# Optimization experiments

Hardware: AMD Instinct MI355X
Metric: run time of the kernel (lower is better)

## Reference

```python
import jax, jax.numpy as jnp
import numpy as np

B, CH, T, D = 16, 64, 2048, 1  # d must be 1 (tf.squeeze(x, axis=-1))
F = 8  # conv filters


def setup_inputs() -> dict:
    key = jax.random.key(0)
    k1, k2, k3, k4 = jax.random.split(key, 4)
    return {
        "x": jax.random.normal(k1, (B, CH, T, D), dtype=jnp.float32),
        "w1": jax.random.normal(k2, (D, F), dtype=jnp.float32) * 0.1,
        "b1": jnp.zeros((F,), dtype=jnp.float32),
        "w2": jax.random.normal(k3, (D, F), dtype=jnp.float32) * 0.1,
        "b2": jnp.zeros((F,), dtype=jnp.float32),
        "gamma": jax.random.normal(k4, (1,), dtype=jnp.float32) * 0.1,
    }


def reference(x, w1, b1, w2, b2, gamma):
    b, ch, t, d = x.shape
    # 1x1 Conv2D == per-position matmul over channel dim; then Permute((2,1,3)) + Reshape((t,-1))
    q = (jnp.matmul(x, w1) + b1)  # (b, ch, t, F)
    k = (jnp.matmul(x, w2) + b2)  # (b, ch, t, F)
    q = jnp.transpose(q, (0, 2, 1, 3)).reshape(b, t, ch * q.shape[-1])  # (b, t, ch*F)
    k = jnp.transpose(k, (0, 2, 1, 3)).reshape(b, t, ch * k.shape[-1])  # (b, t, ch*F)
    energy = jnp.einsum('btf,bsf->bts', q, k)  # (b, t, t)
    max_h = jnp.max(energy, axis=2, keepdims=True)
    min_h = jnp.min(energy, axis=2, keepdims=True)
    energy = (energy - min_h) / (max_h - min_h + 1e-8)
    attention = jax.nn.softmax(energy, axis=-1)  # (b, t, t)
    x_sq = x[..., 0]  # (b, ch, t)
    # matmul(x_sq, attention, transpose_b=True): out[b,c,i] = sum_j x_sq[b,c,j] * attention[b,i,j]
    mixed = jnp.einsum('bcj,bij->bci', x_sq, attention)  # (b, ch, t)
    return gamma[0] * mixed[..., None] + x  # (b, ch, t, 1)
```

## Files before the change

### kernel.cpp

```cpp
#include <hip/hip_runtime.h>

#define NB 16
#define NCH 64
#define NT 2048
#define TI 64
#define TJ 64
#define STR 72

typedef __attribute__((ext_vector_type(8))) short bf8;
typedef __attribute__((ext_vector_type(4))) float f4;

static __device__ __forceinline__ short f2b(float f) {
    unsigned u = __float_as_uint(f);
    u += 0x7fffu + ((u >> 16) & 1u);
    return (short)(u >> 16);
}

__global__ __launch_bounds__(256)
void prep_k(const float* __restrict__ x, float* __restrict__ Xs, short* __restrict__ xT) {
    __shared__ float T[NCH][65];
    const int b = blockIdx.y, t0 = blockIdx.x * 64;
    const int tid = threadIdx.x;
    const float* xb = x + (size_t)b * NCH * NT;

    const int tt = (tid & 15) * 4;
    #pragma unroll
    for (int co = 0; co < 4; ++co) {
        int c = co * 16 + (tid >> 4);
        float4 v = *reinterpret_cast<const float4*>(&xb[(size_t)c * NT + t0 + tt]);
        T[c][tt] = v.x; T[c][tt + 1] = v.y; T[c][tt + 2] = v.z; T[c][tt + 3] = v.w;
    }
    __syncthreads();
    if (tid < 64) {
        float s = 0.f;
        #pragma unroll
        for (int c = 0; c < NCH; ++c) s += T[c][tid];
        Xs[b * NT + t0 + tid] = s;
    }
    const int row = tid >> 2, cs = (tid & 3) * 16;
    bf8 v0, v1;
    #pragma unroll
    for (int u = 0; u < 8; ++u) v0[u] = f2b(T[cs + u][row]);
    #pragma unroll
    for (int u = 0; u < 8; ++u) v1[u] = f2b(T[cs + 8 + u][row]);
    short* dst = xT + ((size_t)b * NT + t0 + row) * NCH + cs;
    *reinterpret_cast<bf8*>(dst) = v0;
    *reinterpret_cast<bf8*>(dst + 8) = v1;
}

__global__ __launch_bounds__(256)
void attn2_k(const float* __restrict__ x,
             const float* __restrict__ w1, const float* __restrict__ b1p,
             const float* __restrict__ w2, const float* __restrict__ b2p,
             const float* __restrict__ gp,
             const float* __restrict__ Xs, const short* __restrict__ xT,
             float* __restrict__ out) {
    __shared__ short xiT[TI][STR];
    __shared__ short xjT[TJ][STR];
    __shared__ short xjn[NCH][STR];
    __shared__ short P[TI][STR];
    __shared__ float XjL[TJ];
    __shared__ float rowSumL[TI];

    const int b  = blockIdx.y;
    const int i0 = blockIdx.x * TI;
    const int tid  = threadIdx.x;
    const int wid  = tid >> 6;
    const int lane = tid & 63;
    const int lq   = lane >> 4;
    const int ln   = lane & 15;

    float s11 = 0.f, s1b2 = 0.f, s2b1 = 0.f, sbb = 0.f;
    #pragma unroll
    for (int f = 0; f < 8; ++f) {
        s11  += w1[f] * w2[f];
        s1b2 += w1[f] * b2p[f];
        s2b1 += b1p[f] * w2[f];
        sbb  += b1p[f] * b2p[f];
    }
    const float c0 = (float)NCH * sbb;
    const float g  = gp[0];

    const short* xTb = xT + (size_t)b * NT * NCH;
    const float* xb  = x + (size_t)b * NCH * NT;

    {
        const int row = tid >> 2, cs = (tid & 3) * 16;
        const bf8* src = reinterpret_cast<const bf8*>(xTb + (size_t)(i0 + row) * NCH + cs);
        bf8* dst = reinterpret_cast<bf8*>(&xiT[row][cs]);
        dst[0] = src[0];
        dst[1] = src[1];
    }

    float XiV[4];
    #pragma unroll
    for (int r = 0; r < 4; ++r) XiV[r] = Xs[b * NT + i0 + wid * 16 + lq * 4 + r];

    float rmin[4], rmax[4];
    #pragma unroll
    for (int r = 0; r < 4; ++r) { rmin[r] = 3.0e38f; rmax[r] = -3.0e38f; }

    for (int j0 = 0; j0 < NT; j0 += TJ) {
        __syncthreads();
        {
            const int row = tid >> 2, cs = (tid & 3) * 16;
            const bf8* src = reinterpret_cast<const bf8*>(xTb + (size_t)(j0 + row) * NCH + cs);
            bf8* dst = reinterpret_cast<bf8*>(&xjT[row][cs]);
            dst[0] = src[0];
            dst[1] = src[1];
        }
        if (tid < 16)
            reinterpret_cast<float4*>(XjL)[tid] =
                reinterpret_cast<const float4*>(Xs + b * NT + j0)[tid];
        __syncthreads();

        bf8 a0 = *reinterpret_cast<const bf8*>(&xiT[wid * 16 + ln][lq * 8]);
        bf8 a1 = *reinterpret_cast<const bf8*>(&xiT[wid * 16 + ln][32 + lq * 8]);
        #pragma unroll
        for (int nb = 0; nb < 4; ++nb) {
            bf8 bb0 = *reinterpret_cast<const bf8*>(&xjT[nb * 16 + ln][lq * 8]);
            bf8 bb1 = *reinterpret_cast<const bf8*>(&xjT[nb * 16 + ln][32 + lq * 8]);
            f4 gacc = {0.f, 0.f, 0.f, 0.f};
            gacc = __builtin_amdgcn_mfma_f32_16x16x32_bf16(a0, bb0, gacc, 0, 0, 0);
            gacc = __builtin_amdgcn_mfma_f32_16x16x32_bf16(a1, bb1, gacc, 0, 0, 0);
            const float xjv = XjL[nb * 16 + ln];
            #pragma unroll
            for (int r = 0; r < 4; ++r) {
                float e = fmaf(s11, gacc[r], fmaf(s1b2, XiV[r], fmaf(s2b1, xjv, c0)));
                rmin[r] = fminf(rmin[r], e);
                rmax[r] = fmaxf(rmax[r], e);
            }
        }
    }

    #pragma unroll
    for (int d = 1; d < 16; d <<= 1) {
        #pragma unroll
        for (int r = 0; r < 4; ++r) {
            rmin[r] = fminf(rmin[r], __shfl_xor(rmin[r], d, 64));
            rmax[r] = fmaxf(rmax[r], __shfl_xor(rmax[r], d, 64));
        }
    }
    float mn[4], inv[4];
    #pragma unroll
    for (int r = 0; r < 4; ++r) {
        mn[r]  = rmin[r];
        inv[r] = 1.f / (rmax[r] - rmin[r] + 1e-8f);
    }

    f4 macc[4];
    #pragma unroll
    for (int nb = 0; nb < 4; ++nb) macc[nb] = (f4){0.f, 0.f, 0.f, 0.f};
    float ps[4] = {0.f, 0.f, 0.f, 0.f};

    for (int j0 = 0; j0 < NT; j0 += TJ) {
        __syncthreads();
        {
            const int row = tid >> 2, cs = (tid & 3) * 16;
            const bf8* src = reinterpret_cast<const bf8*>(xTb + (size_t)(j0 + row) * NCH + cs);
            bf8* dst = reinterpret_cast<bf8*>(&xjT[row][cs]);
            dst[0] = src[0];
            dst[1] = src[1];
        }
        {
            const int c = tid >> 2, js = (tid & 3) * 16;
            const float* s = &xb[(size_t)c * NT + j0 + js];
            float4 f0 = *reinterpret_cast<const float4*>(s);
            float4 f1 = *reinterpret_cast<const float4*>(s + 4);
            float4 fA = *reinterpret_cast<const float4*>(s + 8);
            float4 fB = *reinterpret_cast<const float4*>(s + 12);
            bf8 v0, v1;
            v0[0] = f2b(f0.x); v0[1] = f2b(f0.y); v0[2] = f2b(f0.z); v0[3] = f2b(f0.w);
            v0[4] = f2b(f1.x); v0[5] = f2b(f1.y); v0[6] = f2b(f1.z); v0[7] = f2b(f1.w);
            v1[0] = f2b(fA.x); v1[1] = f2b(fA.y); v1[2] = f2b(fA.z); v1[3] = f2b(fA.w);
            v1[4] = f2b(fB.x); v1[5] = f2b(fB.y); v1[6] = f2b(fB.z); v1[7] = f2b(fB.w);
            *reinterpret_cast<bf8*>(&xjn[c][js])     = v0;
            *reinterpret_cast<bf8*>(&xjn[c][js + 8]) = v1;
        }
        if (tid < 16)
            reinterpret_cast<float4*>(XjL)[tid] =
                reinterpret_cast<const float4*>(Xs + b * NT + j0)[tid];
        __syncthreads();

        bf8 a0 = *reinterpret_cast<const bf8*>(&xiT[wid * 16 + ln][lq * 8]);
        bf8 a1 = *reinterpret_cast<const bf8*>(&xiT[wid * 16 + ln][32 + lq * 8]);
        #pragma unroll
        for (int nb = 0; nb < 4; ++nb) {
            bf8 bb0 = *reinterpret_cast<const bf8*>(&xjT[nb * 16 + ln][lq * 8]);
            bf8 bb1 = *reinterpret_cast<const bf8*>(&xjT[nb * 16 + ln][32 + lq * 8]);
            f4 gacc = {0.f, 0.f, 0.f, 0.f};
            gacc = __builtin_amdgcn_mfma_f32_16x16x32_bf16(a0, bb0, gacc, 0, 0, 0);
            gacc = __builtin_amdgcn_mfma_f32_16x16x32_bf16(a1, bb1, gacc, 0, 0, 0);
            const float xjv = XjL[nb * 16 + ln];
            #pragma unroll
            for (int r = 0; r < 4; ++r) {
                float e = fmaf(s11, gacc[r], fmaf(s1b2, XiV[r], fmaf(s2b1, xjv, c0)));
                float p = __expf((e - mn[r]) * inv[r]);
                ps[r] += p;
                P[wid * 16 + lq * 4 + r][nb * 16 + ln] = f2b(p);
            }
        }
        __syncthreads();

        bf8 ma0 = *reinterpret_cast<const bf8*>(&xjn[wid * 16 + ln][lq * 8]);
        bf8 ma1 = *reinterpret_cast<const bf8*>(&xjn[wid * 16 + ln][32 + lq * 8]);
        #pragma unroll
        for (int nb = 0; nb < 4; ++nb) {
            bf8 pb0 = *reinterpret_cast<const bf8*>(&P[nb * 16 + ln][lq * 8]);
            bf8 pb1 = *reinterpret_cast<const bf8*>(&P[nb * 16 + ln][32 + lq * 8]);
            macc[nb] = __builtin_amdgcn_mfma_f32_16x16x32_bf16(ma0, pb0, macc[nb], 0, 0, 0);
            macc[nb] = __builtin_amdgcn_mfma_f32_16x16x32_bf16(ma1, pb1, macc[nb], 0, 0, 0);
        }
    }

    #pragma unroll
    for (int d = 1; d < 16; d <<= 1)
        #pragma unroll
        for (int r = 0; r < 4; ++r) ps[r] += __shfl_xor(ps[r], d, 64);
    if (ln == 0) {
        #pragma unroll
        for (int r = 0; r < 4; ++r) rowSumL[wid * 16 + lq * 4 + r] = ps[r];
    }
    __syncthreads();

    #pragma unroll
    for (int nb = 0; nb < 4; ++nb) {
        const int i = i0 + nb * 16 + ln;
        const float rs = rowSumL[nb * 16 + ln];
        #pragma unroll
        for (int r = 0; r < 4; ++r) {
            const int c = wid * 16 + lq * 4 + r;
            const size_t off = ((size_t)b * NCH + c) * NT + i;
            out[off] = g * macc[nb][r] / rs + xb[(size_t)c * NT + i];
        }
    }
}

extern "C" void kernel_launch(void* const* d_in, const int* in_sizes, int n_in,
                              void* d_out, int out_size, void* d_ws, size_t ws_size,
                              hipStream_t stream) {
    const float* x     = (const float*)d_in[0];
    const float* w1    = (const float*)d_in[1];
    const float* b1    = (const float*)d_in[2];
    const float* w2    = (const float*)d_in[3];
    const float* b2    = (const float*)d_in[4];
    const float* gamma = (const float*)d_in[5];
    float* out = (float*)d_out;

    float* Xs = (float*)d_ws;
    short* xT = (short*)((char*)d_ws + (size_t)NB * NT * 4);

    hipLaunchKernelGGL(prep_k, dim3(NT / 64, NB), dim3(256), 0, stream, x, Xs, xT);
    hipLaunchKernelGGL(attn2_k, dim3(NT / TI, NB), dim3(256), 0, stream,
                       x, w1, b1, w2, b2, gamma, Xs, xT, out);
}
```

Baseline: 111.1 us.

## Halve row tile, split key columns across waves, precompute bf16 x in prep

Shrinks the query tile from 64 to 32 rows, which doubles the grid to 1024 blocks. Each wave now owns a 16-column slice of the key tile instead of a 16-row slice, so row min/max and row sums need a cross-wave LDS reduction with extra barriers. The prep kernel also writes a bf16 copy of x in channel-major layout, so the attention loop loads it directly instead of converting fp32 on every j-tile in every block. The goal is better occupancy and less redundant conversion work. The cost is re-reading all keys for twice as many blocks and more synchronisation.

```diff
diff --git a/kernel.cpp b/kernel.cpp
--- a/kernel.cpp
+++ b/kernel.cpp
@@ -3,11 +3,12 @@
 #define NB 16
 #define NCH 64
 #define NT 2048
-#define TI 64
+#define TI 32
 #define TJ 64
 #define STR 72
 
 typedef __attribute__((ext_vector_type(8))) short bf8;
+typedef __attribute__((ext_vector_type(4))) short bf4;
 typedef __attribute__((ext_vector_type(4))) float f4;
 
 static __device__ __forceinline__ short f2b(float f) {
@@ -17,7 +18,8 @@
 }
 
 __global__ __launch_bounds__(256)
-void prep_k(const float* __restrict__ x, float* __restrict__ Xs, short* __restrict__ xT) {
+void prep_k(const float* __restrict__ x, float* __restrict__ Xs,
+            short* __restrict__ xT, short* __restrict__ xn) {
     __shared__ float T[NCH][65];
     const int b = blockIdx.y, t0 = blockIdx.x * 64;
     const int tid = threadIdx.x;
@@ -29,6 +31,8 @@
         int c = co * 16 + (tid >> 4);
         float4 v = *reinterpret_cast<const float4*>(&xb[(size_t)c * NT + t0 + tt]);
         T[c][tt] = v.x; T[c][tt + 1] = v.y; T[c][tt + 2] = v.z; T[c][tt + 3] = v.w;
+        bf4 w; w[0] = f2b(v.x); w[1] = f2b(v.y); w[2] = f2b(v.z); w[3] = f2b(v.w);
+        *reinterpret_cast<bf4*>(&xn[((size_t)b * NCH + c) * NT + t0 + tt]) = w;
     }
     __syncthreads();
     if (tid < 64) {
@@ -49,18 +53,20 @@
 }
 
 __global__ __launch_bounds__(256)
-void attn2_k(const float* __restrict__ x,
+void attn3_k(const float* __restrict__ x,
              const float* __restrict__ w1, const float* __restrict__ b1p,
              const float* __restrict__ w2, const float* __restrict__ b2p,
              const float* __restrict__ gp,
              const float* __restrict__ Xs, const short* __restrict__ xT,
+             const short* __restrict__ xn,
              float* __restrict__ out) {
     __shared__ short xiT[TI][STR];
     __shared__ short xjT[TJ][STR];
     __shared__ short xjn[NCH][STR];
     __shared__ short P[TI][STR];
     __shared__ float XjL[TJ];
-    __shared__ float rowSumL[TI];
+    __shared__ float redA[4][TI], redB[4][TI];
+    __shared__ float rowMinL[TI], rowMaxL[TI], rowSumL[TI];
 
     const int b  = blockIdx.y;
     const int i0 = blockIdx.x * TI;
@@ -82,23 +88,27 @@
     const float g  = gp[0];
 
     const short* xTb = xT + (size_t)b * NT * NCH;
+    const short* xnb = xn + (size_t)b * NCH * NT;
     const float* xb  = x + (size_t)b * NCH * NT;
 
     {
-        const int row = tid >> 2, cs = (tid & 3) * 16;
-        const bf8* src = reinterpret_cast<const bf8*>(xTb + (size_t)(i0 + row) * NCH + cs);
-        bf8* dst = reinterpret_cast<bf8*>(&xiT[row][cs]);
-        dst[0] = src[0];
-        dst[1] = src[1];
-    }
-
-    float XiV[4];
-    #pragma unroll
-    for (int r = 0; r < 4; ++r) XiV[r] = Xs[b * NT + i0 + wid * 16 + lq * 4 + r];
-
-    float rmin[4], rmax[4];
-    #pragma unroll
-    for (int r = 0; r < 4; ++r) { rmin[r] = 3.0e38f; rmax[r] = -3.0e38f; }
+        const int row = tid >> 3, cs = (tid & 7) * 8;
+        *reinterpret_cast<bf8*>(&xiT[row][cs]) =
+            *reinterpret_cast<const bf8*>(xTb + (size_t)(i0 + row) * NCH + cs);
+    }
+
+    float XiV[2][4];
+    #pragma unroll
+    for (int mb = 0; mb < 2; ++mb)
+        #pragma unroll
+        for (int r = 0; r < 4; ++r)
+            XiV[mb][r] = Xs[b * NT + i0 + mb * 16 + lq * 4 + r];
+
+    float rmin[2][4], rmax[2][4];
+    #pragma unroll
+    for (int mb = 0; mb < 2; ++mb)
+        #pragma unroll
+        for (int r = 0; r < 4; ++r) { rmin[mb][r] = 3.0e38f; rmax[mb][r] = -3.0e38f; }
 
     for (int j0 = 0; j0 < NT; j0 += TJ) {
         __syncthreads();
@@ -114,44 +124,69 @@
                 reinterpret_cast<const float4*>(Xs + b * NT + j0)[tid];
         __syncthreads();
 
-        bf8 a0 = *reinterpret_cast<const bf8*>(&xiT[wid * 16 + ln][lq * 8]);
-        bf8 a1 = *reinterpret_cast<const bf8*>(&xiT[wid * 16 + ln][32 + lq * 8]);
-        #pragma unroll
-        for (int nb = 0; nb < 4; ++nb) {
-            bf8 bb0 = *reinterpret_cast<const bf8*>(&xjT[nb * 16 + ln][lq * 8]);
-            bf8 bb1 = *reinterpret_cast<const bf8*>(&xjT[nb * 16 + ln][32 + lq * 8]);
+        bf8 b0 = *reinterpret_cast<const bf8*>(&xjT[wid * 16 + ln][lq * 8]);
+        bf8 b1 = *reinterpret_cast<const bf8*>(&xjT[wid * 16 + ln][32 + lq * 8]);
+        const float xjv = XjL[wid * 16 + ln];
+        #pragma unroll
+        for (int mb = 0; mb < 2; ++mb) {
+            bf8 a0 = *reinterpret_cast<const bf8*>(&xiT[mb * 16 + ln][lq * 8]);
+            bf8 a1 = *reinterpret_cast<const bf8*>(&xiT[mb * 16 + ln][32 + lq * 8]);
             f4 gacc = {0.f, 0.f, 0.f, 0.f};
-            gacc = __builtin_amdgcn_mfma_f32_16x16x32_bf16(a0, bb0, gacc, 0, 0, 0);
-            gacc = __builtin_amdgcn_mfma_f32_16x16x32_bf16(a1, bb1, gacc, 0, 0, 0);
-            const float xjv = XjL[nb * 16 + ln];
-            #pragma unroll
-            for (int r = 0; r < 4; ++r) {
-                float e = fmaf(s11, gacc[r], fmaf(s1b2, XiV[r], fmaf(s2b1, xjv, c0)));
-                rmin[r] = fminf(rmin[r], e);
-                rmax[r] = fmaxf(rmax[r], e);
-            }
-        }
-    }
-
-    #pragma unroll
-    for (int d = 1; d < 16; d <<= 1) {
+            gacc = __builtin_amdgcn_mfma_f32_16x16x32_bf16(a0, b0, gacc, 0, 0, 0);
+            gacc = __builtin_amdgcn_mfma_f32_16x16x32_bf16(a1, b1, gacc, 0, 0, 0);
+            #pragma unroll
+            for (int r = 0; r < 4; ++r) {
+                float e = fmaf(s11, gacc[r], fmaf(s1b2, XiV[mb][r], fmaf(s2b1, xjv, c0)));
+                rmin[mb][r] = fminf(rmin[mb][r], e);
+                rmax[mb][r] = fmaxf(rmax[mb][r], e);
+            }
+        }
+    }
+
+    #pragma unroll
+    for (int d = 1; d < 16; d <<= 1)
+        #pragma unroll
+        for (int mb = 0; mb < 2; ++mb)
+            #pragma unroll
+            for (int r = 0; r < 4; ++r) {
+                rmin[mb][r] = fminf(rmin[mb][r], __shfl_xor(rmin[mb][r], d, 64));
+                rmax[mb][r] = fmaxf(rmax[mb][r], __shfl_xor(rmax[mb][r], d, 64));
+            }
+    if (ln == 0)
+        #pragma unroll
+        for (int mb = 0; mb < 2; ++mb)
+            #pragma unroll
+            for (int r = 0; r < 4; ++r) {
+                redA[wid][mb * 16 + lq * 4 + r] = rmin[mb][r];
+                redB[wid][mb * 16 + lq * 4 + r] = rmax[mb][r];
+            }
+    __syncthreads();
+    if (tid < TI) {
+        float a = redA[0][tid], bb = redB[0][tid];
+        #pragma unroll
+        for (int w = 1; w < 4; ++w) {
+            a  = fminf(a, redA[w][tid]);
+            bb = fmaxf(bb, redB[w][tid]);
+        }
+        rowMinL[tid] = a;
+        rowMaxL[tid] = bb;
+    }
+    __syncthreads();
+
+    float mn[2][4], inv[2][4];
+    #pragma unroll
+    for (int mb = 0; mb < 2; ++mb)
         #pragma unroll
         for (int r = 0; r < 4; ++r) {
-            rmin[r] = fminf(rmin[r], __shfl_xor(rmin[r], d, 64));
-            rmax[r] = fmaxf(rmax[r], __shfl_xor(rmax[r], d, 64));
-        }
-    }
-    float mn[4], inv[4];
-    #pragma unroll
-    for (int r = 0; r < 4; ++r) {
-        mn[r]  = rmin[r];
-        inv[r] = 1.f / (rmax[r] - rmin[r] + 1e-8f);
-    }
-
-    f4 macc[4];
-    #pragma unroll
-    for (int nb = 0; nb < 4; ++nb) macc[nb] = (f4){0.f, 0.f, 0.f, 0.f};
-    float ps[4] = {0.f, 0.f, 0.f, 0.f};
+            const int i = mb * 16 + lq * 4 + r;
+            mn[mb][r]  = rowMinL[i];
+            inv[mb][r] = 1.f / (rowMaxL[i] - rowMinL[i] + 1e-8f);
+        }
+
+    f4 macc[2];
+    macc[0] = (f4){0.f, 0.f, 0.f, 0.f};
+    macc[1] = (f4){0.f, 0.f, 0.f, 0.f};
+    float ps[2][4] = {};
 
     for (int j0 = 0; j0 < NT; j0 += TJ) {
         __syncthreads();
@@ -161,43 +196,32 @@
             bf8* dst = reinterpret_cast<bf8*>(&xjT[row][cs]);
             dst[0] = src[0];
             dst[1] = src[1];
-        }
-        {
-            const int c = tid >> 2, js = (tid & 3) * 16;
-            const float* s = &xb[(size_t)c * NT + j0 + js];
-            float4 f0 = *reinterpret_cast<const float4*>(s);
-            float4 f1 = *reinterpret_cast<const float4*>(s + 4);
-            float4 fA = *reinterpret_cast<const float4*>(s + 8);
-            float4 fB = *reinterpret_cast<const float4*>(s + 12);
-            bf8 v0, v1;
-            v0[0] = f2b(f0.x); v0[1] = f2b(f0.y); v0[2] = f2b(f0.z); v0[3] = f2b(f0.w);
-            v0[4] = f2b(f1.x); v0[5] = f2b(f1.y); v0[6] = f2b(f1.z); v0[7] = f2b(f1.w);
-            v1[0] = f2b(fA.x); v1[1] = f2b(fA.y); v1[2] = f2b(fA.z); v1[3] = f2b(fA.w);
-            v1[4] = f2b(fB.x); v1[5] = f2b(fB.y); v1[6] = f2b(fB.z); v1[7] = f2b(fB.w);
-            *reinterpret_cast<bf8*>(&xjn[c][js])     = v0;
-            *reinterpret_cast<bf8*>(&xjn[c][js + 8]) = v1;
+            const bf8* src2 = reinterpret_cast<const bf8*>(xnb + (size_t)row * NT + j0 + (tid & 3) * 16);
+            bf8* dst2 = reinterpret_cast<bf8*>(&xjn[row][(tid & 3) * 16]);
+            dst2[0] = src2[0];
+            dst2[1] = src2[1];
         }
         if (tid < 16)
             reinterpret_cast<float4*>(XjL)[tid] =
                 reinterpret_cast<const float4*>(Xs + b * NT + j0)[tid];
         __syncthreads();
 
-        bf8 a0 = *reinterpret_cast<const bf8*>(&xiT[wid * 16 + ln][lq * 8]);
-        bf8 a1 = *reinterpret_cast<const bf8*>(&xiT[wid * 16 + ln][32 + lq * 8]);
-        #pragma unroll
-        for (int nb = 0; nb < 4; ++nb) {
-            bf8 bb0 = *reinterpret_cast<const bf8*>(&xjT[nb * 16 + ln][lq * 8]);
-            bf8 bb1 = *reinterpret_cast<const bf8*>(&xjT[nb * 16 + ln][32 + lq * 8]);
+        bf8 b0 = *reinterpret_cast<const bf8*>(&xjT[wid * 16 + ln][lq * 8]);
+        bf8 b1 = *reinterpret_cast<const bf8*>(&xjT[wid * 16 + ln][32 + lq * 8]);
+        const float xjv = XjL[wid * 16 + ln];
+        #pragma unroll
+        for (int mb = 0; mb < 2; ++mb) {
+            bf8 a0 = *reinterpret_cast<const bf8*>(&xiT[mb * 16 + ln][lq * 8]);
+            bf8 a1 = *reinterpret_cast<const bf8*>(&xiT[mb * 16 + ln][32 + lq * 8]);
             f4 gacc = {0.f, 0.f, 0.f, 0.f};
-            gacc = __builtin_amdgcn_mfma_f32_16x16x32_bf16(a0, bb0, gacc, 0, 0, 0);
-            gacc = __builtin_amdgcn_mfma_f32_16x16x32_bf16(a1, bb1, gacc, 0, 0, 0);
-            const float xjv = XjL[nb * 16 + ln];
-            #pragma unroll
-            for (int r = 0; r < 4; ++r) {
-                float e = fmaf(s11, gacc[r], fmaf(s1b2, XiV[r], fmaf(s2b1, xjv, c0)));
-                float p = __expf((e - mn[r]) * inv[r]);
-                ps[r] += p;
-                P[wid * 16 + lq * 4 + r][nb * 16 + ln] = f2b(p);
+            gacc = __builtin_amdgcn_mfma_f32_16x16x32_bf16(a0, b0, gacc, 0, 0, 0);
+            gacc = __builtin_amdgcn_mfma_f32_16x16x32_bf16(a1, b1, gacc, 0, 0, 0);
+            #pragma unroll
+            for (int r = 0; r < 4; ++r) {
+                float e = fmaf(s11, gacc[r], fmaf(s1b2, XiV[mb][r], fmaf(s2b1, xjv, c0)));
+                float p = __expf((e - mn[mb][r]) * inv[mb][r]);
+                ps[mb][r] += p;
+                P[mb * 16 + lq * 4 + r][wid * 16 + ln] = f2b(p);
             }
         }
         __syncthreads();
@@ -205,7 +229,7 @@
         bf8 ma0 = *reinterpret_cast<const bf8*>(&xjn[wid * 16 + ln][lq * 8]);
         bf8 ma1 = *reinterpret_cast<const bf8*>(&xjn[wid * 16 + ln][32 + lq * 8]);
         #pragma unroll
-        for (int nb = 0; nb < 4; ++nb) {
+        for (int nb = 0; nb < 2; ++nb) {
             bf8 pb0 = *reinterpret_cast<const bf8*>(&P[nb * 16 + ln][lq * 8]);
             bf8 pb1 = *reinterpret_cast<const bf8*>(&P[nb * 16 + ln][32 + lq * 8]);
             macc[nb] = __builtin_amdgcn_mfma_f32_16x16x32_bf16(ma0, pb0, macc[nb], 0, 0, 0);
@@ -216,15 +240,27 @@
     #pragma unroll
     for (int d = 1; d < 16; d <<= 1)
         #pragma unroll
-        for (int r = 0; r < 4; ++r) ps[r] += __shfl_xor(ps[r], d, 64);
-    if (ln == 0) {
-        #pragma unroll
-        for (int r = 0; r < 4; ++r) rowSumL[wid * 16 + lq * 4 + r] = ps[r];
-    }
-    __syncthreads();
-
-    #pragma unroll
-    for (int nb = 0; nb < 4; ++nb) {
+        for (int mb = 0; mb < 2; ++mb)
+            #pragma unroll
+            for (int r = 0; r < 4; ++r)
+                ps[mb][r] += __shfl_xor(ps[mb][r], d, 64);
+    if (ln == 0)
+        #pragma unroll
+        for (int mb = 0; mb < 2; ++mb)
+            #pragma unroll
+            for (int r = 0; r < 4; ++r)
+                redA[wid][mb * 16 + lq * 4 + r] = ps[mb][r];
+    __syncthreads();
+    if (tid < TI) {
+        float s = 0.f;
+        #pragma unroll
+        for (int w = 0; w < 4; ++w) s += redA[w][tid];
+        rowSumL[tid] = s;
+    }
+    __syncthreads();
+
+    #pragma unroll
+    for (int nb = 0; nb < 2; ++nb) {
         const int i = i0 + nb * 16 + ln;
         const float rs = rowSumL[nb * 16 + ln];
         #pragma unroll
@@ -249,8 +285,10 @@
 
     float* Xs = (float*)d_ws;
     short* xT = (short*)((char*)d_ws + (size_t)NB * NT * 4);
-
-    hipLaunchKernelGGL(prep_k, dim3(NT / 64, NB), dim3(256), 0, stream, x, Xs, xT);
-    hipLaunchKernelGGL(attn2_k, dim3(NT / TI, NB), dim3(256), 0, stream,
-                       x, w1, b1, w2, b2, gamma, Xs, xT, out);
-}
+    short* xn = (short*)((char*)d_ws + (size_t)NB * NT * 4
+                         + (size_t)NB * NT * NCH * 2);
+
+    hipLaunchKernelGGL(prep_k, dim3(NT / 64, NB), dim3(256), 0, stream, x, Xs, xT, xn);
+    hipLaunchKernelGGL(attn3_k, dim3(NT / TI, NB), dim3(256), 0, stream,
+                       x, w1, b1, w2, b2, gamma, Xs, xT, xn, out);
+}
```

Measured after the change: 100.3 us. 1.11x faster.
